# Kernel tuning notes

Measured on AMD Instinct MI355X. Metric: run time of the kernel, lower is better.

## Reference

```python
import jax, jax.numpy as jnp
import numpy as np

DIM = 96
HEADS = 6
WS = 8                      # window_size
OWS = int(WS * 0.5) + WS    # overlap_win_size = 12
PAD = (OWS - WS) // 2       # 2
Dd = Hh = Ww = 24
B = 1
L = Dd * Hh * Ww
MLP_H = DIM * 2
TBL = (WS + OWS - 1) ** 3   # 6859 relative-position-bias entries


def setup_inputs() -> dict:
    key = jax.random.key(0)
    ks = jax.random.split(key, 8)
    def n(k, shape, s=0.02):
        return jax.random.normal(k, shape, jnp.float32) * s
    return {
        "x": jax.random.normal(ks[0], (B, L, DIM), jnp.float32),
        "ln1_w": jnp.ones((DIM,), jnp.float32),
        "ln1_b": jnp.zeros((DIM,), jnp.float32),
        "qkv_w": n(ks[1], (3 * DIM, DIM)),
        "qkv_b": jnp.zeros((3 * DIM,), jnp.float32),
        "rpb": n(ks[2], (TBL, HEADS)),
        "proj_w": n(ks[3], (DIM, DIM)),
        "proj_b": jnp.zeros((DIM,), jnp.float32),
        "ln2_w": jnp.ones((DIM,), jnp.float32),
        "ln2_b": jnp.zeros((DIM,), jnp.float32),
        "fc1_w": n(ks[4], (MLP_H, DIM)),
        "fc1_b": jnp.zeros((MLP_H,), jnp.float32),
        "fc2_w": n(ks[5], (DIM, MLP_H)),
        "fc2_b": jnp.zeros((DIM,), jnp.float32),
        "rpi": jax.random.randint(ks[6], (WS ** 3, OWS ** 3), 0, TBL),
        "D": Dd, "H": Hh, "W": Ww,
    }


def _ln(x, w, b):
    m = jnp.mean(x, -1, keepdims=True)
    v = jnp.var(x, -1, keepdims=True)
    return (x - m) / jnp.sqrt(v + 1e-5) * w + b


def _ocab3d(x, ln1_w, ln1_b, qkv_w, qkv_b, rpb, proj_w, proj_b,
            ln2_w, ln2_b, fc1_w, fc1_b, fc2_w, fc2_b, rpi, D, H, W):
    Bz, Lz, C = x.shape
    hd = C // HEADS
    scale = hd ** -0.5
    shortcut = x

    xn = _ln(x, ln1_w, ln1_b).reshape(Bz, D, H, W, C)
    qkv = xn @ qkv_w.T + qkv_b                   # [B,D,H,W,3C]
    q = qkv[..., :C]
    kv = qkv[..., C:]                            # cat(k, v) on channels, [B,D,H,W,2C]

    nD, nH, nW = D // WS, H // WS, W // WS
    nw = nD * nH * nW

    # non-overlapping query windows -> [B*nw, WS^3, C]
    qw = q.reshape(Bz, nD, WS, nH, WS, nW, WS, C)
    qw = qw.transpose(0, 1, 3, 5, 2, 4, 6, 7).reshape(Bz * nw, WS ** 3, C)

    # overlapping kv windows via pad + strided gather (mirrors F.pad + unfold)
    kvp = jnp.pad(kv, ((0, 0), (PAD, PAD), (PAD, PAD), (PAD, PAD), (0, 0)))
    idx_d = (jnp.arange(nD) * WS)[:, None] + jnp.arange(OWS)[None, :]
    idx_h = (jnp.arange(nH) * WS)[:, None] + jnp.arange(OWS)[None, :]
    idx_w = (jnp.arange(nW) * WS)[:, None] + jnp.arange(OWS)[None, :]
    kw = kvp[:, idx_d]                 # [B,nD,OWS,Hp,Wp,2C]
    kw = kw[:, :, :, idx_h]            # [B,nD,OWS,nH,OWS,Wp,2C]
    kw = kw[:, :, :, :, :, idx_w]      # [B,nD,OWS,nH,OWS,nW,OWS,2C]
    kw = kw.transpose(0, 1, 3, 5, 2, 4, 6, 7).reshape(Bz * nw, OWS ** 3, 2 * C)
    kk, vv = kw[..., :C], kw[..., C:]

    qh = qw.reshape(-1, WS ** 3, HEADS, hd).transpose(0, 2, 1, 3) * scale
    kh = kk.reshape(-1, OWS ** 3, HEADS, hd).transpose(0, 2, 1, 3)
    vh = vv.reshape(-1, OWS ** 3, HEADS, hd).transpose(0, 2, 1, 3)

    attn = jnp.einsum('bhqd,bhkd->bhqk', qh, kh)               # [B*nw,H,512,1728]
    bias = rpb[rpi.reshape(-1)].reshape(WS ** 3, OWS ** 3, HEADS).transpose(2, 0, 1)
    attn = jax.nn.softmax(attn + bias[None], axis=-1)
    out = jnp.einsum('bhqk,bhkd->bhqd', attn, vh)
    out = out.transpose(0, 2, 1, 3).reshape(Bz * nw, WS ** 3, C)

    # window reverse -> [B, L, C]
    out = out.reshape(Bz, nD, nH, nW, WS, WS, WS, C)
    out = out.transpose(0, 1, 4, 2, 5, 3, 6, 7).reshape(Bz, D * H * W, C)

    x2 = out @ proj_w.T + proj_b + shortcut
    h1 = jax.nn.gelu(_ln(x2, ln2_w, ln2_b) @ fc1_w.T + fc1_b, approximate=False)
    return x2 + (h1 @ fc2_w.T + fc2_b)


def reference(x, ln1_w, ln1_b, qkv_w, qkv_b, rpb, proj_w, proj_b,
              ln2_w, ln2_b, fc1_w, fc1_b, fc2_w, fc2_b, rpi, D, H, W):
    return _ocab3d(x, ln1_w, ln1_b, qkv_w, qkv_b, rpb, proj_w, proj_b,
                   ln2_w, ln2_b, fc1_w, fc1_b, fc2_w, fc2_b, rpi, D, H, W)
```

## Files before the change

### kernel.cpp

```cpp
#include <hip/hip_runtime.h>
#include <math.h>

#define DIMC   96
#define NHEADS 6
#define HD     16
#define WSZ    8
#define OWSZ   12
#define PADW   2
#define DD     24
#define LTOK   13824
#define NWIN   27
#define NKEY   1728
#define NROW   512
#define MLPH   192
#define PDIM   28
#define PD3    21952
#define KVPN   (NHEADS*PD3*32)
#define TBL    6859
#define LSTR   82944
#define AOSTR  1327104

typedef __attribute__((ext_vector_type(4))) short bf16x4;
typedef __attribute__((ext_vector_type(8))) short bf16x8;
typedef __attribute__((ext_vector_type(4))) float f32x4;

__device__ __forceinline__ unsigned short bfround(float f) {
    unsigned u = __float_as_uint(f);
    return (unsigned short)((u + 0x7FFFu + ((u >> 16) & 1u)) >> 16);
}
__device__ __forceinline__ unsigned bfpack(float a, float b) {
    unsigned ua = __float_as_uint(a), ub = __float_as_uint(b);
    ua = (ua + 0x7FFFu + ((ua >> 16) & 1u)) >> 16;
    ub = (ub + 0x7FFFu + ((ub >> 16) & 1u)) >> 16;
    return ua | (ub << 16);
}
__device__ __forceinline__ uint4 pack8(const float* v) {
    uint4 u;
    u.x = bfpack(v[0], v[1]); u.y = bfpack(v[2], v[3]);
    u.z = bfpack(v[4], v[5]); u.w = bfpack(v[6], v[7]);
    return u;
}
__device__ __forceinline__ bf16x4 pack4(f32x4 p) {
    union { uint2 u; bf16x4 v; } r;
    r.u.x = __builtin_amdgcn_perm(__float_as_uint(p[1]), __float_as_uint(p[0]), 0x07060302u);
    r.u.y = __builtin_amdgcn_perm(__float_as_uint(p[3]), __float_as_uint(p[2]), 0x07060302u);
    return r.v;
}
__device__ __forceinline__ f32x4 mfma16(bf16x4 a, bf16x4 b, f32x4 c) {
#if __has_builtin(__builtin_amdgcn_mfma_f32_16x16x16bf16_1k)
    return __builtin_amdgcn_mfma_f32_16x16x16bf16_1k(a, b, c, 0, 0, 0);
#else
    bf16x8 a8 = {a[0], a[1], a[2], a[3], 0, 0, 0, 0};
    bf16x8 b8 = {b[0], b[1], b[2], b[3], 0, 0, 0, 0};
    return __builtin_amdgcn_mfma_f32_16x16x32_bf16(a8, b8, c, 0, 0, 0);
#endif
}

#define ZBLK 2058
__global__ __launch_bounds__(256) void init_kernel(
        float4* __restrict__ kvz, const float* __restrict__ rpb,
        float* __restrict__ rpbT) {
    int bx = blockIdx.x;
    if (bx < ZBLK) {
        int i = bx * 256 + threadIdx.x;
        if (i < KVPN * 2 / 16) kvz[i] = make_float4(0.f, 0.f, 0.f, 0.f);
    } else {
        int i = (bx - ZBLK) * 256 + threadIdx.x;
        if (i < TBL) {
            #pragma unroll
            for (int h = 0; h < NHEADS; ++h) rpbT[h * TBL + i] = rpb[i * NHEADS + h];
        }
    }
}

template<int KT>
__global__ __launch_bounds__(256) void qkv_kernel(
        const float* __restrict__ X, const float* __restrict__ W,
        const float* __restrict__ bias, const float* __restrict__ lnw,
        const float* __restrict__ lnb,
        unsigned short* __restrict__ out, unsigned short* __restrict__ out2) {
    __shared__ uint4 Af4[2 * KT * 4 * 16];
    __shared__ uint4 Bf4[6 * KT * 4 * 16];
    int tid  = threadIdx.x;
    int nc   = blockIdx.x % 3;
    int row0 = (blockIdx.x / 3) * 32;

    if (tid < 128) {
        int row = tid >> 2, part = tid & 3;
        int rt = row >> 4, mm = row & 15;
        float v[24];
        const float4* xp = (const float4*)(X + (long)(row0 + row) * 96 + part * 24);
        float s = 0.f, sq = 0.f;
        #pragma unroll
        for (int i = 0; i < 6; ++i) {
            float4 t = xp[i];
            v[i*4+0] = t.x; v[i*4+1] = t.y; v[i*4+2] = t.z; v[i*4+3] = t.w;
            s  += t.x + t.y + t.z + t.w;
            sq += t.x*t.x + t.y*t.y + t.z*t.z + t.w*t.w;
        }
        s  += __shfl_xor(s, 1);  s  += __shfl_xor(s, 2);
        sq += __shfl_xor(sq, 1); sq += __shfl_xor(sq, 2);
        float mean = s * (1.f / 96.f);
        float inv  = rsqrtf(sq * (1.f / 96.f) - mean * mean + 1e-5f);
        const float4* wp = (const float4*)(lnw + part * 24);
        const float4* bp = (const float4*)(lnb + part * 24);
        #pragma unroll
        for (int i = 0; i < 6; ++i) {
            float4 wv = wp[i], bv = bp[i];
            v[i*4+0] = (v[i*4+0] - mean) * inv * wv.x + bv.x;
            v[i*4+1] = (v[i*4+1] - mean) * inv * wv.y + bv.y;
            v[i*4+2] = (v[i*4+2] - mean) * inv * wv.z + bv.z;
            v[i*4+3] = (v[i*4+3] - mean) * inv * wv.w + bv.w;
        }
        #pragma unroll
        for (int gg = 0; gg < 3; ++gg) {
            int g = part * 3 + gg;
            int kt = g >> 2, qq = g & 3;
            Af4[((rt * KT + kt) * 4 + qq) * 16 + mm] = pack8(v + gg * 8);
        }
    }
    for (int idx = tid; idx < 96 * 4 * KT; idx += 256) {
        int n = idx / (4 * KT);
        int g = idx % (4 * KT);
        const float4* wp = (const float4*)(W + (long)(nc * 96 + n) * 96 + g * 8);
        float v[8];
        float4 t0 = wp[0], t1 = wp[1];
        v[0]=t0.x; v[1]=t0.y; v[2]=t0.z; v[3]=t0.w;
        v[4]=t1.x; v[5]=t1.y; v[6]=t1.z; v[7]=t1.w;
        int ct = n >> 4, nn = n & 15, kt = g >> 2, qg = g & 3;
        Bf4[((ct * KT + kt) * 4 + qg) * 16 + nn] = pack8(v);
    }
    __syncthreads();

    int wave = tid >> 6, lane = tid & 63;
    int qq = lane >> 4, mI = lane & 15;
    int rt = wave & 1, cg = wave >> 1;

    f32x4 acc[3];
    #pragma unroll
    for (int j = 0; j < 3; ++j) acc[j] = (f32x4){0.f, 0.f, 0.f, 0.f};
    #pragma unroll
    for (int kt = 0; kt < KT; ++kt) {
        bf16x8 a = *(const bf16x8*)&Af4[((rt * KT + kt) * 4 + qq) * 16 + mI];
        #pragma unroll
        for (int j = 0; j < 3; ++j) {
            bf16x8 b = *(const bf16x8*)&Bf4[(((cg * 3 + j) * KT + kt) * 4 + qq) * 16 + mI];
            acc[j] = __builtin_amdgcn_mfma_f32_16x16x32_bf16(a, b, acc[j], 0, 0, 0);
        }
    }

    float bv[3];
    #pragma unroll
    for (int j = 0; j < 3; ++j) bv[j] = bias[nc * 96 + (cg * 3 + j) * 16 + mI];
    #pragma unroll
    for (int r = 0; r < 4; ++r) {
        int row = row0 + rt * 16 + qq * 4 + r;
        if (nc == 0) {
            unsigned short* op = out + (long)row * 96;
            #pragma unroll
            for (int j = 0; j < 3; ++j)
                op[(cg * 3 + j) * 16 + mI] = bfround(0.25f * (acc[j][r] + bv[j]));
        } else {
            int d = row / 576, hh = (row / 24) % 24, w2 = row % 24;
            long pos = ((long)(d + 2) * 28 + (hh + 2)) * 28 + (w2 + 2);
            #pragma unroll
            for (int j = 0; j < 3; ++j) {
                int head = cg * 3 + j;
                out2[((long)head * PD3 + pos) * 32 +
                     (nc == 2 ? 16 : 0) + mI] = bfround(acc[j][r] + bv[j]);
            }
        }
    }
}

__global__ __launch_bounds__(256) void bias_kernel(
        const int* __restrict__ rpi, const float* __restrict__ rpbT,
        unsigned short* __restrict__ biasP) {
    int bx = blockIdx.x;
    int head = bx / 216;
    int r2 = bx % 216;
    int kt = r2 >> 1, qh = r2 & 1;
    const float* tab = rpbT + head * TBL;
    int k0 = kt * 16;
    int qi = qh * 256 + threadIdx.x;
    const int* rp = rpi + (long)qi * NKEY + k0;
    int idx[16];
    #pragma unroll
    for (int j = 0; j < 4; ++j) {
        int4 t = *(const int4*)(rp + j * 4);
        idx[j*4+0] = t.x; idx[j*4+1] = t.y; idx[j*4+2] = t.z; idx[j*4+3] = t.w;
    }
    #pragma unroll
    for (int quad = 0; quad < 4; ++quad) {
        ushort4 v;
        v.x = bfround(tab[idx[quad*4+0]]);
        v.y = bfround(tab[idx[quad*4+1]]);
        v.z = bfround(tab[idx[quad*4+2]]);
        v.w = bfround(tab[idx[quad*4+3]]);
        *(ushort4*)(biasP + ((((long)head*108 + kt)*4 + quad)*512 + qi)*4) = v;
    }
}

#define KSTR 20
#define VSTR 68
__global__ __launch_bounds__(256) void attn_kernel(
        const unsigned short* __restrict__ q, const unsigned short* __restrict__ kvp2,
        const unsigned short* __restrict__ biasP, float* __restrict__ ao,
        float* __restrict__ lbuf) {
    __shared__ unsigned short Ks[2][64 * KSTR];
    __shared__ unsigned short Vs[2][16 * VSTR];
    int bid = blockIdx.x;
    int xcd = bid & 7, slot = bid >> 3;
    int L = xcd * 162 + slot;
    int head = L / 216;
    int rem = L % 216;
    int half = rem / 108;
    int r3 = rem % 108;
    int quart = r3 / 27;
    int w = r3 % 27;
    int wd8 = (w / 9) * 8, wh8 = ((w / 3) % 3) * 8, ww8 = (w % 3) * 8;
    int tid = threadIdx.x, wave = tid >> 6, lane = tid & 63;
    int quad = lane >> 4, m16 = lane & 15;
    int key = tid >> 2, part = tid & 3;
    int c0 = half ? 13 : 0;
    int cn = half ? 14 : 13;

    auto kvaddr = [&](int c) -> const uint4* {
        int jg = c * 64 + key;
        int i = jg / 144, jh = (jg / 12) % 12, jw = jg % 12;
        long sp = ((long)(wd8 + i) * PDIM + (wh8 + jh)) * PDIM + (ww8 + jw);
        return (const uint4*)(kvp2 + ((long)head * PD3 + sp) * 32 + part * 8);
    };
    auto writeLDS = [&](int b, uint4 v) {
        if (part < 2) {
            *(uint2*)(&Ks[b][key * KSTR + part * 8])     = make_uint2(v.x, v.y);
            *(uint2*)(&Ks[b][key * KSTR + part * 8 + 4]) = make_uint2(v.z, v.w);
        } else {
            int d0 = (part - 2) * 8;
            Vs[b][(d0+0)*VSTR + key] = (unsigned short)(v.x);
            Vs[b][(d0+1)*VSTR + key] = (unsigned short)(v.x >> 16);
            Vs[b][(d0+2)*VSTR + key] = (unsigned short)(v.y);
            Vs[b][(d0+3)*VSTR + key] = (unsigned short)(v.y >> 16);
            Vs[b][(d0+4)*VSTR + key] = (unsigned short)(v.z);
            Vs[b][(d0+5)*VSTR + key] = (unsigned short)(v.z >> 16);
            Vs[b][(d0+6)*VSTR + key] = (unsigned short)(v.w);
            Vs[b][(d0+7)*VSTR + key] = (unsigned short)(v.w >> 16);
        }
    };

    int grow[2]; bf16x4 qf[2];
    #pragma unroll
    for (int qt = 0; qt < 2; ++qt) {
        int ql = quart * 128 + wave * 32 + qt * 16 + m16;
        int ld = ql >> 6, lh = (ql >> 3) & 7, lw = ql & 7;
        grow[qt] = ((wd8 + ld) * 24 + (wh8 + lh)) * 24 + (ww8 + lw);
        qf[qt] = *(const bf16x4*)(q + (long)grow[qt] * 96 + head * 16 + quad * 4);
    }

    const unsigned short* bbase = biasP + (long)head * 884736 + quad * 2048
                                  + ((quart * 128 + wave * 32 + m16) << 2);
    uint2 bcur[2][4];
    #pragma unroll
    for (int qt = 0; qt < 2; ++qt)
        #pragma unroll
        for (int kt = 0; kt < 4; ++kt)
            bcur[qt][kt] = *(const uint2*)(bbase + (long)(c0*4 + kt) * 8192 + qt * 64);

    writeLDS(0, *kvaddr(c0));

    f32x4 o[2];
    o[0] = (f32x4){0.f,0.f,0.f,0.f}; o[1] = (f32x4){0.f,0.f,0.f,0.f};
    float l[2] = {0.f, 0.f};
    uint4 stgn;

    #pragma unroll 1
    for (int cc = 0; cc < cn; ++cc) {
        int c = c0 + cc;
        if (cc + 1 < cn) stgn = *kvaddr(c + 1);
        __syncthreads();
        int b = cc & 1;

        bf16x4 kf[4];
        #pragma unroll
        for (int kt = 0; kt < 4; ++kt)
            kf[kt] = *(const bf16x4*)(&Ks[b][(kt * 16 + m16) * KSTR + quad * 4]);

        f32x4 S[2][4];
        #pragma unroll
        for (int qt = 0; qt < 2; ++qt)
            #pragma unroll
            for (int kt = 0; kt < 4; ++kt) {
                uint2 bv = bcur[qt][kt];
                f32x4 ci;
                ci[0] = __uint_as_float(bv.x << 16);
                ci[1] = __uint_as_float(bv.x & 0xffff0000u);
                ci[2] = __uint_as_float(bv.y << 16);
                ci[3] = __uint_as_float(bv.y & 0xffff0000u);
                S[qt][kt] = mfma16(kf[kt], qf[qt], ci);
            }

        uint2 bnxt[2][4];
        if (cc + 1 < cn) {
            const unsigned short* bp = bbase + (long)(c + 1) * 32768;
            #pragma unroll
            for (int qt = 0; qt < 2; ++qt)
                #pragma unroll
                for (int kt = 0; kt < 4; ++kt)
                    bnxt[qt][kt] = *(const uint2*)(bp + kt * 8192 + qt * 64);
        }

        #pragma unroll
        for (int qt = 0; qt < 2; ++qt) {
            float ls = 0.f;
            #pragma unroll
            for (int kt = 0; kt < 4; ++kt)
                #pragma unroll
                for (int r = 0; r < 4; ++r) {
                    float p = __expf(S[qt][kt][r]);
                    S[qt][kt][r] = p; ls += p;
                }
            l[qt] += ls;
        }

        #pragma unroll
        for (int kt = 0; kt < 4; ++kt) {
            bf16x4 vf = *(const bf16x4*)(&Vs[b][m16 * VSTR + kt * 16 + quad * 4]);
            o[0] = mfma16(vf, pack4(S[0][kt]), o[0]);
            o[1] = mfma16(vf, pack4(S[1][kt]), o[1]);
        }

        if (cc + 1 < cn) writeLDS((cc + 1) & 1, stgn);
        #pragma unroll
        for (int qt = 0; qt < 2; ++qt)
            #pragma unroll
            for (int kt = 0; kt < 4; ++kt) bcur[qt][kt] = bnxt[qt][kt];
    }

    float* aout = ao + (long)half * AOSTR;
    float* lout = lbuf + (long)half * LSTR;
    #pragma unroll
    for (int qt = 0; qt < 2; ++qt) {
        float lq = l[qt];
        lq += __shfl_xor(lq, 16);
        lq += __shfl_xor(lq, 32);
        float4* op = (float4*)(aout + (long)grow[qt] * 96 + head * 16 + quad * 4);
        *op = make_float4(o[qt][0], o[qt][1], o[qt][2], o[qt][3]);
        if (quad == 0) lout[grow[qt] * 6 + head] = lq;
    }
}

__global__ __launch_bounds__(256) void mlp_kernel(
        const float* __restrict__ ao0, const float* __restrict__ ao1,
        const float* __restrict__ lbuf,
        const float* __restrict__ projw, const float* __restrict__ projb,
        const float* __restrict__ x,
        const float* __restrict__ ln2w, const float* __restrict__ ln2b,
        const float* __restrict__ fc1w, const float* __restrict__ fc1b,
        const float* __restrict__ fc2w, const float* __restrict__ fc2b,
        float* __restrict__ out) {
    __shared__ uint4 Af4[2 * 3 * 4 * 16];
    __shared__ uint4 Bf4[6 * 3 * 4 * 16];
    __shared__ float x2s[32 * 96];
    __shared__ unsigned short h16[32 * 192];
    int tid = threadIdx.x;
    int row0 = blockIdx.x * 32;
    int wave = tid >> 6, lane = tid & 63;
    int qq = lane >> 4, mI = lane & 15;
    int rt = wave & 1, cg = wave >> 1;

    if (tid < 128) {
        int row = tid >> 2, part = tid & 3;
        int rtA = row >> 4, mm = row & 15;
        int grow = row0 + row;
        const float4* a0 = (const float4*)(ao0 + (long)grow * 96 + part * 24);
        const float4* a1 = (const float4*)(ao1 + (long)grow * 96 + part * 24);
        int ha = (part * 3) >> 1, hb = ha + 1;
        float inva = 1.f / (lbuf[grow*6 + ha] + lbuf[LSTR + grow*6 + ha]);
        float invb = 1.f / (lbuf[grow*6 + hb] + lbuf[LSTR + grow*6 + hb]);
        float v[24];
        #pragma unroll
        for (int i = 0; i < 6; ++i) {
            float4 u0 = a0[i], u1 = a1[i];
            #pragma unroll
            for (int j = 0; j < 4; ++j) {
                int gc = part * 24 + i * 4 + j;
                float lv = ((gc >> 4) == ha) ? inva : invb;
                float s = (j==0?u0.x+u1.x : j==1?u0.y+u1.y : j==2?u0.z+u1.z : u0.w+u1.w);
                v[i*4+j] = s * lv;
            }
        }
        #pragma unroll
        for (int gg = 0; gg < 3; ++gg) {
            int g = part * 3 + gg;
            int kt = g >> 2, q4 = g & 3;
            Af4[((rtA * 3 + kt) * 4 + q4) * 16 + mm] = pack8(v + gg * 8);
        }
    }
    for (int idx = tid; idx < 96 * 12; idx += 256) {
        int n = idx / 12, g = idx % 12;
        const float4* wp = (const float4*)(projw + (long)n * 96 + g * 8);
        float v[8];
        float4 t0 = wp[0], t1 = wp[1];
        v[0]=t0.x; v[1]=t0.y; v[2]=t0.z; v[3]=t0.w;
        v[4]=t1.x; v[5]=t1.y; v[6]=t1.z; v[7]=t1.w;
        int ct = n >> 4, nn = n & 15, kt = g >> 2, qg = g & 3;
        Bf4[((ct * 3 + kt) * 4 + qg) * 16 + nn] = pack8(v);
    }
    __syncthreads();

    {
        f32x4 acc[3];
        #pragma unroll
        for (int j = 0; j < 3; ++j) acc[j] = (f32x4){0.f,0.f,0.f,0.f};
        #pragma unroll
        for (int kt = 0; kt < 3; ++kt) {
            bf16x8 a = *(const bf16x8*)&Af4[((rt * 3 + kt) * 4 + qq) * 16 + mI];
            #pragma unroll
            for (int j = 0; j < 3; ++j) {
                bf16x8 b = *(const bf16x8*)&Bf4[(((cg * 3 + j) * 3 + kt) * 4 + qq) * 16 + mI];
                acc[j] = __builtin_amdgcn_mfma_f32_16x16x32_bf16(a, b, acc[j], 0, 0, 0);
            }
        }
        float bv[3];
        #pragma unroll
        for (int j = 0; j < 3; ++j) bv[j] = projb[(cg * 3 + j) * 16 + mI];
        #pragma unroll
        for (int r = 0; r < 4; ++r) {
            int row = rt * 16 + qq * 4 + r;
            int grow = row0 + row;
            #pragma unroll
            for (int j = 0; j < 3; ++j) {
                int col = (cg * 3 + j) * 16 + mI;
                x2s[row * 96 + col] = acc[j][r] + bv[j] + x[(long)grow * 96 + col];
            }
        }
    }
    __syncthreads();

    if (tid < 128) {
        int row = tid >> 2, part = tid & 3;
        int rtA = row >> 4, mm = row & 15;
        float v[24];
        const float4* xp = (const float4*)(x2s + row * 96 + part * 24);
        float s = 0.f, sq = 0.f;
        #pragma unroll
        for (int i = 0; i < 6; ++i) {
            float4 t = xp[i];
            v[i*4+0] = t.x; v[i*4+1] = t.y; v[i*4+2] = t.z; v[i*4+3] = t.w;
            s  += t.x + t.y + t.z + t.w;
            sq += t.x*t.x + t.y*t.y + t.z*t.z + t.w*t.w;
        }
        s  += __shfl_xor(s, 1);  s  += __shfl_xor(s, 2);
        sq += __shfl_xor(sq, 1); sq += __shfl_xor(sq, 2);
        float mean = s * (1.f / 96.f);
        float inv  = rsqrtf(sq * (1.f / 96.f) - mean * mean + 1e-5f);
        const float4* wp = (const float4*)(ln2w + part * 24);
        const float4* bp = (const float4*)(ln2b + part * 24);
        #pragma unroll
        for (int i = 0; i < 6; ++i) {
            float4 wv = wp[i], bv = bp[i];
            v[i*4+0] = (v[i*4+0] - mean) * inv * wv.x + bv.x;
            v[i*4+1] = (v[i*4+1] - mean) * inv * wv.y + bv.y;
            v[i*4+2] = (v[i*4+2] - mean) * inv * wv.z + bv.z;
            v[i*4+3] = (v[i*4+3] - mean) * inv * wv.w + bv.w;
        }
        #pragma unroll
        for (int gg = 0; gg < 3; ++gg) {
            int g = part * 3 + gg;
            int kt = g >> 2, q4 = g & 3;
            Af4[((rtA * 3 + kt) * 4 + q4) * 16 + mm] = pack8(v + gg * 8);
        }
    }

    #pragma unroll 1
    for (int nc = 0; nc < 2; ++nc) {
        if (nc) __syncthreads();
        for (int idx = tid; idx < 96 * 12; idx += 256) {
            int n = idx / 12, g = idx % 12;
            const float4* wp = (const float4*)(fc1w + (long)(nc * 96 + n) * 96 + g * 8);
            float v[8];
            float4 t0 = wp[0], t1 = wp[1];
            v[0]=t0.x; v[1]=t0.y; v[2]=t0.z; v[3]=t0.w;
            v[4]=t1.x; v[5]=t1.y; v[6]=t1.z; v[7]=t1.w;
            int ct = n >> 4, nn = n & 15, kt = g >> 2, qg = g & 3;
            Bf4[((ct * 3 + kt) * 4 + qg) * 16 + nn] = pack8(v);
        }
        __syncthreads();

        f32x4 acc[3];
        #pragma unroll
        for (int j = 0; j < 3; ++j) acc[j] = (f32x4){0.f,0.f,0.f,0.f};
        #pragma unroll
        for (int kt = 0; kt < 3; ++kt) {
            bf16x8 a = *(const bf16x8*)&Af4[((rt * 3 + kt) * 4 + qq) * 16 + mI];
            #pragma unroll
            for (int j = 0; j < 3; ++j) {
                bf16x8 b = *(const bf16x8*)&Bf4[(((cg * 3 + j) * 3 + kt) * 4 + qq) * 16 + mI];
                acc[j] = __builtin_amdgcn_mfma_f32_16x16x32_bf16(a, b, acc[j], 0, 0, 0);
            }
        }
        float bv[3];
        #pragma unroll
        for (int j = 0; j < 3; ++j) bv[j] = fc1b[nc * 96 + (cg * 3 + j) * 16 + mI];
        #pragma unroll
        for (int r = 0; r < 4; ++r) {
            int row = rt * 16 + qq * 4 + r;
            #pragma unroll
            for (int j = 0; j < 3; ++j) {
                int col = nc * 96 + (cg * 3 + j) * 16 + mI;
                float v = acc[j][r] + bv[j];
                float g = 0.5f * v * (1.f + erff(v * 0.70710678f));
                int fi = (((row >> 4) * 6 + (col >> 5)) * 4 + ((col >> 3) & 3)) * 16 + (row & 15);
                h16[fi * 8 + (col & 7)] = bfround(g);
            }
        }
    }

    f32x4 acc2[3];
    #pragma unroll
    for (int j = 0; j < 3; ++j) acc2[j] = (f32x4){0.f,0.f,0.f,0.f};
    #pragma unroll 1
    for (int kh = 0; kh < 2; ++kh) {
        __syncthreads();
        for (int idx = tid; idx < 96 * 12; idx += 256) {
            int n = idx / 12, g = idx % 12;
            const float4* wp = (const float4*)(fc2w + (long)n * 192 + kh * 96 + g * 8);
            float v[8];
            float4 t0 = wp[0], t1 = wp[1];
            v[0]=t0.x; v[1]=t0.y; v[2]=t0.z; v[3]=t0.w;
            v[4]=t1.x; v[5]=t1.y; v[6]=t1.z; v[7]=t1.w;
            int ct = n >> 4, nn = n & 15, kt = g >> 2, qg = g & 3;
            Bf4[((ct * 3 + kt) * 4 + qg) * 16 + nn] = pack8(v);
        }
        __syncthreads();
        #pragma unroll
        for (int kt = 0; kt < 3; ++kt) {
            int ktA = kh * 3 + kt;
            bf16x8 a = *(const bf16x8*)&h16[(((rt * 6 + ktA) * 4 + qq) * 16 + mI) * 8];
            #pragma unroll
            for (int j = 0; j < 3; ++j) {
                bf16x8 b = *(const bf16x8*)&Bf4[(((cg * 3 + j) * 3 + kt) * 4 + qq) * 16 + mI];
                acc2[j] = __builtin_amdgcn_mfma_f32_16x16x32_bf16(a, b, acc2[j], 0, 0, 0);
            }
        }
    }
    float bv[3];
    #pragma unroll
    for (int j = 0; j < 3; ++j) bv[j] = fc2b[(cg * 3 + j) * 16 + mI];
    #pragma unroll
    for (int r = 0; r < 4; ++r) {
        int row = rt * 16 + qq * 4 + r;
        int grow = row0 + row;
        #pragma unroll
        for (int j = 0; j < 3; ++j) {
            int col = (cg * 3 + j) * 16 + mI;
            out[(long)grow * 96 + col] = acc2[j][r] + bv[j] + x2s[row * 96 + col];
        }
    }
}

extern "C" void kernel_launch(void* const* d_in, const int* in_sizes, int n_in,
                              void* d_out, int out_size, void* d_ws, size_t ws_size,
                              hipStream_t stream) {
    const float* x     = (const float*)d_in[0];
    const float* ln1w  = (const float*)d_in[1];
    const float* ln1b  = (const float*)d_in[2];
    const float* qkvw  = (const float*)d_in[3];
    const float* qkvb  = (const float*)d_in[4];
    const float* rpb   = (const float*)d_in[5];
    const float* projw = (const float*)d_in[6];
    const float* projb = (const float*)d_in[7];
    const float* ln2w  = (const float*)d_in[8];
    const float* ln2b  = (const float*)d_in[9];
    const float* fc1w  = (const float*)d_in[10];
    const float* fc1b  = (const float*)d_in[11];
    const float* fc2w  = (const float*)d_in[12];
    const float* fc2b  = (const float*)d_in[13];
    const int*   rpi   = (const int*)d_in[14];
    float* outp = (float*)d_out;

    float* ws = (float*)d_ws;
    float*          aop    = ws;
    unsigned short* q16    = (unsigned short*)(ws + 2654208);
    unsigned short* kvp16  = (unsigned short*)(ws + 3317760);
    unsigned short* biasP  = (unsigned short*)(ws + 5425152);
    float*          rpbT   = ws + 8079360;
    float*          lbuf   = ws + 8120514;

    init_kernel<<<ZBLK + 27, 256, 0, stream>>>((float4*)kvp16, rpb, rpbT);
    qkv_kernel<3><<<1296, 256, 0, stream>>>(x, qkvw, qkvb, ln1w, ln1b, q16, kvp16);
    bias_kernel<<<1296, 256, 0, stream>>>(rpi, rpbT, biasP);
    attn_kernel<<<NWIN * NHEADS * 4 * 2, 256, 0, stream>>>(q16, kvp16, biasP, aop, lbuf);
    mlp_kernel<<<432, 256, 0, stream>>>(aop, aop + AOSTR, lbuf, projw, projb, x,
                                        ln2w, ln2b, fc1w, fc1b, fc2w, fc2b, outp);
}
```

Before: 186.7 us.

## Fuse init, QKV and bias gather into one pre-kernel with fp32 bias

Replaces the separate init, qkv and bias kernels with a single pre_kernel whose blocks interleave QKV projection and relative-position-bias gathering, with a tail of blocks that zero only the padding border of the kv buffer. The bias is gathered straight from rpb in its original layout and stored in fp32, so the transpose pass and bf16 unpacking in the attention inner loop go away. The attention block-to-work mapping also drops the XCD-aware swizzle in favour of a window-major order. This removes two launches and the full zero-fill, but doubles the bias buffer's memory traffic during attention and may lose the L2 locality the swizzle provided.

```diff
diff --git a/kernel.cpp b/kernel.cpp
--- a/kernel.cpp
+++ b/kernel.cpp
@@ -15,7 +15,6 @@
 #define MLPH   192
 #define PDIM   28
 #define PD3    21952
-#define KVPN   (NHEADS*PD3*32)
 #define TBL    6859
 #define LSTR   82944
 #define AOSTR  1327104
@@ -56,34 +55,62 @@
 #endif
 }
 
-#define ZBLK 2058
-__global__ __launch_bounds__(256) void init_kernel(
-        float4* __restrict__ kvz, const float* __restrict__ rpb,
-        float* __restrict__ rpbT) {
-    int bx = blockIdx.x;
-    if (bx < ZBLK) {
-        int i = bx * 256 + threadIdx.x;
-        if (i < KVPN * 2 / 16) kvz[i] = make_float4(0.f, 0.f, 0.f, 0.f);
-    } else {
-        int i = (bx - ZBLK) * 256 + threadIdx.x;
-        if (i < TBL) {
-            #pragma unroll
-            for (int h = 0; h < NHEADS; ++h) rpbT[h * TBL + i] = rpb[i * NHEADS + h];
-        }
-    }
-}
-
-template<int KT>
-__global__ __launch_bounds__(256) void qkv_kernel(
+#define PREQ  2592
+#define NZB   515
+__global__ __launch_bounds__(256) void pre_kernel(
         const float* __restrict__ X, const float* __restrict__ W,
         const float* __restrict__ bias, const float* __restrict__ lnw,
         const float* __restrict__ lnb,
-        unsigned short* __restrict__ out, unsigned short* __restrict__ out2) {
-    __shared__ uint4 Af4[2 * KT * 4 * 16];
-    __shared__ uint4 Bf4[6 * KT * 4 * 16];
-    int tid  = threadIdx.x;
-    int nc   = blockIdx.x % 3;
-    int row0 = (blockIdx.x / 3) * 32;
+        const int* __restrict__ rpi, const float* __restrict__ rpb,
+        unsigned short* __restrict__ q16, unsigned short* __restrict__ kvp2,
+        float* __restrict__ biasP) {
+    __shared__ uint4 Af4[2 * 3 * 4 * 16];
+    __shared__ uint4 Bf4[6 * 3 * 4 * 16];
+    int bx = blockIdx.x, tid = threadIdx.x;
+
+    if (bx >= PREQ) {
+        int t = (bx - PREQ) * 256 + tid;
+        if (t < 21952 * 6) {
+            int head = t / PD3, pos = t % PD3;
+            int d = pos / 784, h = (pos / 28) % 28, w = pos % 28;
+            if (d < 2 || d >= 26 || h < 2 || h >= 26 || w < 2 || w >= 26) {
+                uint4* p = (uint4*)(kvp2 + ((long)head * PD3 + pos) * 32);
+                uint4 z = make_uint4(0, 0, 0, 0);
+                p[0] = z; p[1] = z; p[2] = z; p[3] = z;
+            }
+        }
+        return;
+    }
+
+    if (bx & 1) {
+        int b2 = bx >> 1;
+        int head = b2 / 216;
+        int r2 = b2 % 216;
+        int kt = r2 >> 1, qh = r2 & 1;
+        int k0 = kt * 16;
+        int qi = qh * 256 + tid;
+        const int* rp = rpi + (long)qi * NKEY + k0;
+        int idx[16];
+        #pragma unroll
+        for (int j = 0; j < 4; ++j) {
+            int4 t = *(const int4*)(rp + j * 4);
+            idx[j*4+0] = t.x; idx[j*4+1] = t.y; idx[j*4+2] = t.z; idx[j*4+3] = t.w;
+        }
+        #pragma unroll
+        for (int quad = 0; quad < 4; ++quad) {
+            float4 v;
+            v.x = rpb[idx[quad*4+0] * NHEADS + head];
+            v.y = rpb[idx[quad*4+1] * NHEADS + head];
+            v.z = rpb[idx[quad*4+2] * NHEADS + head];
+            v.w = rpb[idx[quad*4+3] * NHEADS + head];
+            *(float4*)(biasP + ((((long)head*108 + kt)*4 + quad)*512 + qi)*4) = v;
+        }
+        return;
+    }
+
+    int b2 = bx >> 1;
+    int nc   = b2 % 3;
+    int row0 = (b2 / 3) * 32;
 
     if (tid < 128) {
         int row = tid >> 2, part = tid & 3;
@@ -116,19 +143,19 @@
         for (int gg = 0; gg < 3; ++gg) {
             int g = part * 3 + gg;
             int kt = g >> 2, qq = g & 3;
-            Af4[((rt * KT + kt) * 4 + qq) * 16 + mm] = pack8(v + gg * 8);
-        }
-    }
-    for (int idx = tid; idx < 96 * 4 * KT; idx += 256) {
-        int n = idx / (4 * KT);
-        int g = idx % (4 * KT);
+            Af4[((rt * 3 + kt) * 4 + qq) * 16 + mm] = pack8(v + gg * 8);
+        }
+    }
+    for (int idx = tid; idx < 96 * 12; idx += 256) {
+        int n = idx / 12;
+        int g = idx % 12;
         const float4* wp = (const float4*)(W + (long)(nc * 96 + n) * 96 + g * 8);
         float v[8];
         float4 t0 = wp[0], t1 = wp[1];
         v[0]=t0.x; v[1]=t0.y; v[2]=t0.z; v[3]=t0.w;
         v[4]=t1.x; v[5]=t1.y; v[6]=t1.z; v[7]=t1.w;
         int ct = n >> 4, nn = n & 15, kt = g >> 2, qg = g & 3;
-        Bf4[((ct * KT + kt) * 4 + qg) * 16 + nn] = pack8(v);
+        Bf4[((ct * 3 + kt) * 4 + qg) * 16 + nn] = pack8(v);
     }
     __syncthreads();
 
@@ -140,11 +167,11 @@
     #pragma unroll
     for (int j = 0; j < 3; ++j) acc[j] = (f32x4){0.f, 0.f, 0.f, 0.f};
     #pragma unroll
-    for (int kt = 0; kt < KT; ++kt) {
-        bf16x8 a = *(const bf16x8*)&Af4[((rt * KT + kt) * 4 + qq) * 16 + mI];
+    for (int kt = 0; kt < 3; ++kt) {
+        bf16x8 a = *(const bf16x8*)&Af4[((rt * 3 + kt) * 4 + qq) * 16 + mI];
         #pragma unroll
         for (int j = 0; j < 3; ++j) {
-            bf16x8 b = *(const bf16x8*)&Bf4[(((cg * 3 + j) * KT + kt) * 4 + qq) * 16 + mI];
+            bf16x8 b = *(const bf16x8*)&Bf4[(((cg * 3 + j) * 3 + kt) * 4 + qq) * 16 + mI];
             acc[j] = __builtin_amdgcn_mfma_f32_16x16x32_bf16(a, b, acc[j], 0, 0, 0);
         }
     }
@@ -156,7 +183,7 @@
     for (int r = 0; r < 4; ++r) {
         int row = row0 + rt * 16 + qq * 4 + r;
         if (nc == 0) {
-            unsigned short* op = out + (long)row * 96;
+            unsigned short* op = q16 + (long)row * 96;
             #pragma unroll
             for (int j = 0; j < 3; ++j)
                 op[(cg * 3 + j) * 16 + mI] = bfround(0.25f * (acc[j][r] + bv[j]));
@@ -166,38 +193,10 @@
             #pragma unroll
             for (int j = 0; j < 3; ++j) {
                 int head = cg * 3 + j;
-                out2[((long)head * PD3 + pos) * 32 +
+                kvp2[((long)head * PD3 + pos) * 32 +
                      (nc == 2 ? 16 : 0) + mI] = bfround(acc[j][r] + bv[j]);
             }
         }
-    }
-}
-
-__global__ __launch_bounds__(256) void bias_kernel(
-        const int* __restrict__ rpi, const float* __restrict__ rpbT,
-        unsigned short* __restrict__ biasP) {
-    int bx = blockIdx.x;
-    int head = bx / 216;
-    int r2 = bx % 216;
-    int kt = r2 >> 1, qh = r2 & 1;
-    const float* tab = rpbT + head * TBL;
-    int k0 = kt * 16;
-    int qi = qh * 256 + threadIdx.x;
-    const int* rp = rpi + (long)qi * NKEY + k0;
-    int idx[16];
-    #pragma unroll
-    for (int j = 0; j < 4; ++j) {
-        int4 t = *(const int4*)(rp + j * 4);
-        idx[j*4+0] = t.x; idx[j*4+1] = t.y; idx[j*4+2] = t.z; idx[j*4+3] = t.w;
-    }
-    #pragma unroll
-    for (int quad = 0; quad < 4; ++quad) {
-        ushort4 v;
-        v.x = bfround(tab[idx[quad*4+0]]);
-        v.y = bfround(tab[idx[quad*4+1]]);
-        v.z = bfround(tab[idx[quad*4+2]]);
-        v.w = bfround(tab[idx[quad*4+3]]);
-        *(ushort4*)(biasP + ((((long)head*108 + kt)*4 + quad)*512 + qi)*4) = v;
     }
 }
 
@@ -205,19 +204,14 @@
 #define VSTR 68
 __global__ __launch_bounds__(256) void attn_kernel(
         const unsigned short* __restrict__ q, const unsigned short* __restrict__ kvp2,
-        const unsigned short* __restrict__ biasP, float* __restrict__ ao,
+        const float* __restrict__ biasP, float* __restrict__ ao,
         float* __restrict__ lbuf) {
     __shared__ unsigned short Ks[2][64 * KSTR];
     __shared__ unsigned short Vs[2][16 * VSTR];
     int bid = blockIdx.x;
-    int xcd = bid & 7, slot = bid >> 3;
-    int L = xcd * 162 + slot;
-    int head = L / 216;
-    int rem = L % 216;
-    int half = rem / 108;
-    int r3 = rem % 108;
-    int quart = r3 / 27;
-    int w = r3 % 27;
+    int w = bid / 48, rem = bid % 48;
+    int head = rem >> 3;
+    int quart = (rem >> 1) & 3, half = rem & 1;
     int wd8 = (w / 9) * 8, wh8 = ((w / 3) % 3) * 8, ww8 = (w % 3) * 8;
     int tid = threadIdx.x, wave = tid >> 6, lane = tid & 63;
     int quad = lane >> 4, m16 = lane & 15;
@@ -257,14 +251,14 @@
         qf[qt] = *(const bf16x4*)(q + (long)grow[qt] * 96 + head * 16 + quad * 4);
     }
 
-    const unsigned short* bbase = biasP + (long)head * 884736 + quad * 2048
-                                  + ((quart * 128 + wave * 32 + m16) << 2);
-    uint2 bcur[2][4];
+    const float* bbase = biasP + (long)head * 884736 + quad * 2048
+                         + ((quart * 128 + wave * 32 + m16) << 2);
+    f32x4 bcur[2][4];
     #pragma unroll
     for (int qt = 0; qt < 2; ++qt)
         #pragma unroll
         for (int kt = 0; kt < 4; ++kt)
-            bcur[qt][kt] = *(const uint2*)(bbase + (long)(c0*4 + kt) * 8192 + qt * 64);
+            bcur[qt][kt] = *(const f32x4*)(bbase + (long)(c0*4 + kt) * 8192 + qt * 64);
 
     writeLDS(0, *kvaddr(c0));
 
@@ -289,24 +283,17 @@
         #pragma unroll
         for (int qt = 0; qt < 2; ++qt)
             #pragma unroll
-            for (int kt = 0; kt < 4; ++kt) {
-                uint2 bv = bcur[qt][kt];
-                f32x4 ci;
-                ci[0] = __uint_as_float(bv.x << 16);
-                ci[1] = __uint_as_float(bv.x & 0xffff0000u);
-                ci[2] = __uint_as_float(bv.y << 16);
-                ci[3] = __uint_as_float(bv.y & 0xffff0000u);
-                S[qt][kt] = mfma16(kf[kt], qf[qt], ci);
-            }
-
-        uint2 bnxt[2][4];
+            for (int kt = 0; kt < 4; ++kt)
+                S[qt][kt] = mfma16(kf[kt], qf[qt], bcur[qt][kt]);
+
+        f32x4 bnxt[2][4];
         if (cc + 1 < cn) {
-            const unsigned short* bp = bbase + (long)(c + 1) * 32768;
+            const float* bp = bbase + (long)(c + 1) * 32768;
             #pragma unroll
             for (int qt = 0; qt < 2; ++qt)
                 #pragma unroll
                 for (int kt = 0; kt < 4; ++kt)
-                    bnxt[qt][kt] = *(const uint2*)(bp + kt * 8192 + qt * 64);
+                    bnxt[qt][kt] = *(const f32x4*)(bp + kt * 8192 + qt * 64);
         }
 
         #pragma unroll
@@ -583,14 +570,12 @@
     float*          aop    = ws;
     unsigned short* q16    = (unsigned short*)(ws + 2654208);
     unsigned short* kvp16  = (unsigned short*)(ws + 3317760);
-    unsigned short* biasP  = (unsigned short*)(ws + 5425152);
-    float*          rpbT   = ws + 8079360;
-    float*          lbuf   = ws + 8120514;
-
-    init_kernel<<<ZBLK + 27, 256, 0, stream>>>((float4*)kvp16, rpb, rpbT);
-    qkv_kernel<3><<<1296, 256, 0, stream>>>(x, qkvw, qkvb, ln1w, ln1b, q16, kvp16);
-    bias_kernel<<<1296, 256, 0, stream>>>(rpi, rpbT, biasP);
-    attn_kernel<<<NWIN * NHEADS * 4 * 2, 256, 0, stream>>>(q16, kvp16, biasP, aop, lbuf);
+    float*          biasPf = ws + 5425152;
+    float*          lbuf   = ws + 10733568;
+
+    pre_kernel<<<PREQ + NZB, 256, 0, stream>>>(x, qkvw, qkvb, ln1w, ln1b,
+                                               rpi, rpb, q16, kvp16, biasPf);
+    attn_kernel<<<NWIN * NHEADS * 4 * 2, 256, 0, stream>>>(q16, kvp16, biasPf, aop, lbuf);
     mlp_kernel<<<432, 256, 0, stream>>>(aop, aop + AOSTR, lbuf, projw, projb, x,
                                         ln2w, ln2b, fc1w, fc1b, fc2w, fc2b, outp);
 }
```

New measurement: 196.2 us. 1.05x slower.
